# Optimization experiments

Hardware: AMD Instinct MI355X
Metric: run time of the kernel (lower is better)

The kernel has to match this reference:

```python
import jax, jax.numpy as jnp
import numpy as np

B, N, IC, PC, OUT = 2, 4096, 256, 128, 128
BN_EPS = 1e-5


def setup_inputs() -> dict:
    key = jax.random.key(0)
    ks = jax.random.split(key, 6)
    return {
        "point_features": jax.random.normal(ks[0], (B, PC, N), jnp.float32),
        "img_features": jax.random.normal(ks[1], (B, IC, N), jnp.float32),
        "fc2_w": jax.random.normal(ks[2], (PC, IC), jnp.float32) * (1.0 / np.sqrt(IC)),
        "fc2_b": jax.random.normal(ks[3], (PC,), jnp.float32) * 0.01,
        "conv_w": jax.random.normal(ks[4], (OUT, 2 * PC), jnp.float32) * (1.0 / np.sqrt(2 * PC)),
        "conv_b": jax.random.normal(ks[5], (OUT,), jnp.float32) * 0.01,
        "bn_gamma": jnp.ones((OUT,), jnp.float32),
        "bn_beta": jnp.zeros((OUT,), jnp.float32),
        "bn_mean": jnp.zeros((OUT,), jnp.float32),
        "bn_var": jnp.ones((OUT,), jnp.float32),
    }


def reference(point_features, img_features, fc2_w, fc2_b, conv_w, conv_b,
              bn_gamma, bn_beta, bn_mean, bn_var):
    # IA_layer3 (dropout in eval mode -> identity)
    rp = jnp.swapaxes(point_features, 1, 2)            # [B, N, pc]
    ri = jnp.swapaxes(img_features, 1, 2) @ fc2_w.T + fc2_b  # fc2: [B, N, pc]
    scale = 1.0 / np.sqrt(PC).astype(np.float32)

    # scores = rp @ ri^T / sqrt(d); softmax over dim=1 (the rp-token axis)
    s_p = jnp.einsum('bnd,bmd->bnm', rp, ri) * scale   # [B, N, N]
    aw_p = jax.nn.softmax(s_p, axis=1)
    out_p = jnp.einsum('bij,bjd->bid', aw_p, rp)       # [B, N, pc]

    s_i = jnp.einsum('bnd,bmd->bnm', ri, rp) * scale   # [B, N, N]
    aw_i = jax.nn.softmax(s_i, axis=1)
    out_i = jnp.einsum('bij,bjd->bid', aw_i, ri)       # [B, N, pc]

    # fuse: permute to channel-first, concat on channels -> [B, 2*pc, N]
    fusion = jnp.concatenate([jnp.swapaxes(out_p, 1, 2),
                              jnp.swapaxes(out_i, 1, 2)], axis=1)
    # conv1d(k=1) + BN(eval) + ReLU, all per-channel elementwise over N
    y = jnp.einsum('oc,bcn->bon', conv_w, fusion) + conv_b[None, :, None]
    inv_std = jax.lax.rsqrt(bn_var + BN_EPS)
    y = (y - bn_mean[None, :, None]) * (bn_gamma * inv_std)[None, :, None] \
        + bn_beta[None, :, None]
    return jax.nn.relu(y)                              # [B, OUT, N]
```

## Files before the change

### kernel.cpp

```cpp
#include <hip/hip_runtime.h>
#include <math.h>

#define NTOK 4096
#define PCH  128
#define ICH  256
#define OCH  128
#define NB   2
#define SCALEF 0.08838834764831845f

typedef __bf16 bf16_t;
typedef __attribute__((ext_vector_type(8))) __bf16 bf16x8;
typedef __attribute__((ext_vector_type(4))) __bf16 bf16x4;
typedef __attribute__((ext_vector_type(4))) float floatx4;

#define LDK 136
#define LDJ 72

__global__ __launch_bounds__(256) void pack_all(const float* __restrict__ pf,
                                                const float* __restrict__ img,
                                                bf16_t* __restrict__ pfC,
                                                bf16_t* __restrict__ pfT,
                                                bf16_t* __restrict__ imgT)
{
    __shared__ float Ls[64][65];
    const int t = threadIdx.x;
    const int n0 = blockIdx.x * 64, b = blockIdx.z;
    const bool ispf = blockIdx.y < 2;
    const int d0 = ispf ? blockIdx.y * 64 : (blockIdx.y - 2) * 64;
    const float* src = (ispf ? pf + ((size_t)(b * PCH + d0)) * NTOK
                             : img + ((size_t)(b * ICH + d0)) * NTOK) + n0;
#pragma unroll
    for (int p = 0; p < 4; p++) {
        int d = p * 16 + (t >> 4), c = t & 15;
        float4 v = *(const float4*)&src[d * NTOK + c * 4];
        Ls[d][c * 4 + 0] = v.x; Ls[d][c * 4 + 1] = v.y;
        Ls[d][c * 4 + 2] = v.z; Ls[d][c * 4 + 3] = v.w;
        if (ispf) {
            bf16x4 o = { (bf16_t)v.x, (bf16_t)v.y, (bf16_t)v.z, (bf16_t)v.w };
            *(bf16x4*)&pfC[((size_t)(b * PCH + d0 + d)) * NTOK + n0 + c * 4] = o;
        }
    }
    __syncthreads();
#pragma unroll
    for (int p = 0; p < 2; p++) {
        int n = p * 32 + (t >> 3), c = t & 7;
        bf16x8 o;
#pragma unroll
        for (int k = 0; k < 8; k++) o[k] = (bf16_t)Ls[c * 8 + k][n];
        if (ispf)
            *(bf16x8*)&pfT[((size_t)(b * NTOK + n0 + n)) * PCH + d0 + c * 8] = o;
        else
            *(bf16x8*)&imgT[((size_t)(b * NTOK + n0 + n)) * ICH + d0 + c * 8] = o;
    }
}

__global__ __launch_bounds__(256) void fc2_mfma(const bf16_t* __restrict__ imgT,
                                                const float* __restrict__ w,
                                                const float* __restrict__ bias,
                                                bf16_t* __restrict__ riC,
                                                bf16_t* __restrict__ riT,
                                                float* __restrict__ zsums)
{
    const int t = threadIdx.x;
    if (blockIdx.y == 0 && blockIdx.z == 0)
        zsums[blockIdx.x * 256 + t] = 0.f;

    const int n0 = blockIdx.x * 64, pbase = blockIdx.y * 64, b = blockIdx.z;
    const int lane = t & 63, wv = t >> 6, tx = lane & 15, q = lane >> 4;
    const int n = n0 + wv * 16 + tx;
    const bf16_t* trow = imgT + ((size_t)(b * NTOK + n)) * ICH;

    floatx4 acc[4];
#pragma unroll
    for (int ot = 0; ot < 4; ot++) acc[ot] = (floatx4){0.f, 0.f, 0.f, 0.f};

#pragma unroll
    for (int s = 0; s < 8; s++) {
        bf16x8 bf = *(const bf16x8*)&trow[s * 32 + q * 8];
#pragma unroll
        for (int ot = 0; ot < 4; ot++) {
            const float* wr = w + (size_t)(pbase + ot * 16 + tx) * ICH + s * 32 + q * 8;
            float4 x0 = *(const float4*)wr;
            float4 x1 = *(const float4*)(wr + 4);
            bf16x8 af;
            af[0] = (bf16_t)x0.x; af[1] = (bf16_t)x0.y; af[2] = (bf16_t)x0.z; af[3] = (bf16_t)x0.w;
            af[4] = (bf16_t)x1.x; af[5] = (bf16_t)x1.y; af[6] = (bf16_t)x1.z; af[7] = (bf16_t)x1.w;
            acc[ot] = __builtin_amdgcn_mfma_f32_16x16x32_bf16(af, bf, acc[ot], 0, 0, 0);
        }
    }

#pragma unroll
    for (int ot = 0; ot < 4; ot++) {
        bf16x4 tv;
#pragma unroll
        for (int r = 0; r < 4; r++) {
            const int p = pbase + ot * 16 + q * 4 + r;
            float v = acc[ot][r] + bias[p];
            tv[r] = (bf16_t)v;
            riC[((size_t)(b * PCH + p)) * NTOK + n] = (bf16_t)v;
        }
        *(bf16x4*)&riT[((size_t)(b * NTOK + n)) * PCH + pbase + ot * 16 + q * 4] = tv;
    }
}

__global__ __launch_bounds__(256, 4) void stats_mfma(const bf16_t* __restrict__ pfT,
                                                     const bf16_t* __restrict__ riT,
                                                     float* __restrict__ zr,
                                                     float* __restrict__ zc,
                                                     float* __restrict__ fus)
{
    __shared__ bf16_t As[64 * LDK];
    __shared__ float zacc[1024];
    const int t = threadIdx.x;
    const int blk = blockIdx.x;

    {
        float4* f4 = (float4*)fus + ((size_t)blk * 256 + t) * 4;
        f4[0] = float4{0.f, 0.f, 0.f, 0.f};
        f4[1] = float4{0.f, 0.f, 0.f, 0.f};
        f4[2] = float4{0.f, 0.f, 0.f, 0.f};
        f4[3] = float4{0.f, 0.f, 0.f, 0.f};
    }

    const int g = blk & 7, slot = blk >> 3;
    const int b = g & 1, js = g >> 1;
    const bf16_t* At = pfT + (size_t)b * NTOK * PCH;
    const bf16_t* Bt = riT + (size_t)b * NTOK * PCH;
    float* zrow = zr + (size_t)b * NTOK;
    float* zcol = zc + (size_t)b * NTOK;
    const int lane = t & 63, w = t >> 6, tx = lane & 15, q = lane >> 4;
    const int i0 = slot * 64;
    const int jbase = js * 1024;
    const int sr = t >> 4, sc = t & 15;
    const bf16_t* Brow = Bt + (size_t)(jbase + w * 16 + tx) * PCH;

    bf16x8 bcur[4];
#pragma unroll
    for (int s = 0; s < 4; s++)
        bcur[s] = *(const bf16x8*)&Brow[s * 32 + q * 8];
#pragma unroll
    for (int p = 0; p < 4; p++) {
        int i = p * 16 + sr;
        *(uint4*)&As[i * LDK + sc * 8] = *(const uint4*)&At[((size_t)(i0 + i)) * PCH + sc * 8];
    }
    __syncthreads();
    bf16x8 af[4][4];
#pragma unroll
    for (int mt = 0; mt < 4; mt++)
#pragma unroll
        for (int s = 0; s < 4; s++)
            af[mt][s] = *(bf16x8*)&As[(mt * 16 + tx) * LDK + s * 32 + q * 8];

    float racc[4] = {0.f, 0.f, 0.f, 0.f};
    for (int jt = 0; jt < 16; jt++) {
        __builtin_amdgcn_s_barrier();
        floatx4 sacc[4];
#pragma unroll
        for (int mt = 0; mt < 4; mt++) {
            sacc[mt] = (floatx4){0.f, 0.f, 0.f, 0.f};
#pragma unroll
            for (int s = 0; s < 4; s++)
                sacc[mt] = __builtin_amdgcn_mfma_f32_16x16x32_bf16(bcur[s], af[mt][s], sacc[mt], 0, 0, 0);
        }
        if (jt < 15) {
            const bf16_t* bn = Brow + (size_t)(jt + 1) * 64 * PCH;
#pragma unroll
            for (int s = 0; s < 4; s++)
                bcur[s] = *(const bf16x8*)&bn[s * 32 + q * 8];
        }

        float ctmp[4] = {0.f, 0.f, 0.f, 0.f};
#pragma unroll
        for (int mt = 0; mt < 4; mt++)
#pragma unroll
            for (int r = 0; r < 4; r++) {
                float e = __expf(sacc[mt][r] * SCALEF);
                racc[mt] += e;
                ctmp[r]  += e;
            }
#pragma unroll
        for (int r = 0; r < 4; r++) {
            float v = ctmp[r];
            v += __shfl_xor(v, 1); v += __shfl_xor(v, 2);
            v += __shfl_xor(v, 4); v += __shfl_xor(v, 8);
            if (tx == 0) zacc[jt * 64 + w * 16 + q * 4 + r] = v;
        }
    }
#pragma unroll
    for (int mt = 0; mt < 4; mt++) {
        float v = racc[mt];
        v += __shfl_xor(v, 16);
        v += __shfl_xor(v, 32);
        if (q == 0) atomicAdd(&zrow[i0 + mt * 16 + tx], v);
    }
    __syncthreads();
#pragma unroll
    for (int k = 0; k < 4; k++)
        atomicAdd(&zcol[jbase + k * 256 + t], zacc[k * 256 + t]);
}

__global__ __launch_bounds__(256, 3) void attn_mfma(const bf16_t* __restrict__ pfT,
                                                    const bf16_t* __restrict__ riT,
                                                    const bf16_t* __restrict__ pfC,
                                                    const bf16_t* __restrict__ riC,
                                                    const float* __restrict__ zrsum,
                                                    const float* __restrict__ zcsum,
                                                    float* __restrict__ fus)
{
    __shared__ bf16_t As[64 * LDK];
    __shared__ bf16_t Es[2][64 * LDJ];
    const int t = threadIdx.x;
    const int blk = blockIdx.x;
    const int g = (blk & 7) * 2 + ((blk >> 3) >> 6);
    const int slot = (blk >> 3) & 63;
    const int b = g & 1, z = g >> 1;
    const int mode = z >> 2, js = z & 3;
    const bf16_t* At = (mode == 0 ? pfT : riT) + (size_t)b * NTOK * PCH;
    const bf16_t* Bt = (mode == 0 ? riT : pfT) + (size_t)b * NTOK * PCH;
    const bf16_t* Vc = (mode == 0 ? pfC : riC) + (size_t)b * PCH * NTOK;
    const float* wsum = (mode == 0 ? zcsum : zrsum) + (size_t)b * NTOK;
    const int lane = t & 63, w = t >> 6, tx = lane & 15, q = lane >> 4;
    const int i0 = slot * 64;
    const int jbase = js * 1024;
    const int sr = t >> 4, sc = t & 15;
    const bf16_t* Brow = Bt + (size_t)(jbase + w * 16 + tx) * PCH;

    bf16x8 bcur[4];
#pragma unroll
    for (int s = 0; s < 4; s++)
        bcur[s] = *(const bf16x8*)&Brow[s * 32 + q * 8];
    bf16x8 vcur[2][2];
#pragma unroll
    for (int nt = 0; nt < 2; nt++)
#pragma unroll
        for (int s = 0; s < 2; s++)
            vcur[nt][s] = *(const bf16x8*)&Vc[((size_t)(w * 32 + nt * 16 + tx)) * NTOK + jbase + s * 32 + q * 8];
    float4 wv = *(const float4*)&wsum[jbase + w * 16 + q * 4];
    float4 wr4 = {1.f / wv.x, 1.f / wv.y, 1.f / wv.z, 1.f / wv.w};

#pragma unroll
    for (int p = 0; p < 4; p++) {
        int i = p * 16 + sr;
        *(uint4*)&As[i * LDK + sc * 8] = *(const uint4*)&At[((size_t)(i0 + i)) * PCH + sc * 8];
    }
    __syncthreads();
    bf16x8 af[4][4];
#pragma unroll
    for (int mt = 0; mt < 4; mt++)
#pragma unroll
        for (int s = 0; s < 4; s++)
            af[mt][s] = *(bf16x8*)&As[(mt * 16 + tx) * LDK + s * 32 + q * 8];

    floatx4 outacc[4][2];
#pragma unroll
    for (int mt = 0; mt < 4; mt++)
#pragma unroll
        for (int nt = 0; nt < 2; nt++)
            outacc[mt][nt] = (floatx4){0.f, 0.f, 0.f, 0.f};

    for (int jt = 0; jt < 16; jt++) {
        const int cur = jt & 1;
        const int j0 = jbase + jt * 64;

        floatx4 sacc[4];
#pragma unroll
        for (int mt = 0; mt < 4; mt++) {
            sacc[mt] = (floatx4){0.f, 0.f, 0.f, 0.f};
#pragma unroll
            for (int s = 0; s < 4; s++)
                sacc[mt] = __builtin_amdgcn_mfma_f32_16x16x32_bf16(bcur[s], af[mt][s], sacc[mt], 0, 0, 0);
        }
        if (jt < 15) {
            const bf16_t* bn = Brow + (size_t)(jt + 1) * 64 * PCH;
#pragma unroll
            for (int s = 0; s < 4; s++)
                bcur[s] = *(const bf16x8*)&bn[s * 32 + q * 8];
        }

#pragma unroll
        for (int mt = 0; mt < 4; mt++) {
            bf16x4 ev;
#pragma unroll
            for (int r = 0; r < 4; r++)
                ev[r] = (bf16_t)(__expf(sacc[mt][r] * SCALEF) * ((const float*)&wr4)[r]);
            *(bf16x4*)&Es[cur][(mt * 16 + tx) * LDJ + w * 16 + q * 4] = ev;
        }
        float4 wnv;
        if (jt < 15)
            wnv = *(const float4*)&wsum[j0 + 64 + w * 16 + q * 4];

        __syncthreads();

        bf16x8 ef[4][2];
#pragma unroll
        for (int mt = 0; mt < 4; mt++)
#pragma unroll
            for (int s = 0; s < 2; s++)
                ef[mt][s] = *(bf16x8*)&Es[cur][(mt * 16 + tx) * LDJ + s * 32 + q * 8];
#pragma unroll
        for (int nt = 0; nt < 2; nt++)
#pragma unroll
            for (int s = 0; s < 2; s++)
#pragma unroll
                for (int mt = 0; mt < 4; mt++)
                    outacc[mt][nt] = __builtin_amdgcn_mfma_f32_16x16x32_bf16(ef[mt][s], vcur[nt][s], outacc[mt][nt], 0, 0, 0);

        if (jt < 15) {
#pragma unroll
            for (int nt = 0; nt < 2; nt++)
#pragma unroll
                for (int s = 0; s < 2; s++)
                    vcur[nt][s] = *(const bf16x8*)&Vc[((size_t)(w * 32 + nt * 16 + tx)) * NTOK + (j0 + 64) + s * 32 + q * 8];
            wr4 = (float4){1.f / wnv.x, 1.f / wnv.y, 1.f / wnv.z, 1.f / wnv.w};
        }
    }

    float* fo = fus + ((size_t)(b * NTOK + i0)) * 256 + mode * 128 + w * 32;
#pragma unroll
    for (int mt = 0; mt < 4; mt++)
#pragma unroll
        for (int nt = 0; nt < 2; nt++)
#pragma unroll
            for (int r = 0; r < 4; r++)
                atomicAdd(&fo[(mt * 16 + q * 4 + r) * 256 + nt * 16 + tx], outacc[mt][nt][r]);
}

__global__ __launch_bounds__(256) void conv_mfma(const float* __restrict__ fus,
                                                 const float* __restrict__ cw,
                                                 const float* __restrict__ cb,
                                                 const float* __restrict__ g,
                                                 const float* __restrict__ be,
                                                 const float* __restrict__ mu,
                                                 const float* __restrict__ var,
                                                 float* __restrict__ out)
{
    const int t = threadIdx.x;
    const int n0 = blockIdx.x * 64, obase = blockIdx.y * 64, b = blockIdx.z;
    const int lane = t & 63, wv = t >> 6, tx = lane & 15, q = lane >> 4;
    const int n = n0 + wv * 16 + tx;
    const float* frow = fus + ((size_t)(b * NTOK + n)) * 256;

    floatx4 acc[4];
#pragma unroll
    for (int ot = 0; ot < 4; ot++) acc[ot] = (floatx4){0.f, 0.f, 0.f, 0.f};

#pragma unroll
    for (int s = 0; s < 8; s++) {
        float4 f0 = *(const float4*)&frow[s * 32 + q * 8];
        float4 f1 = *(const float4*)&frow[s * 32 + q * 8 + 4];
        bf16x8 bf;
        bf[0] = (bf16_t)f0.x; bf[1] = (bf16_t)f0.y; bf[2] = (bf16_t)f0.z; bf[3] = (bf16_t)f0.w;
        bf[4] = (bf16_t)f1.x; bf[5] = (bf16_t)f1.y; bf[6] = (bf16_t)f1.z; bf[7] = (bf16_t)f1.w;
#pragma unroll
        for (int ot = 0; ot < 4; ot++) {
            const float* wr = cw + (size_t)(obase + ot * 16 + tx) * 256 + s * 32 + q * 8;
            float4 x0 = *(const float4*)wr;
            float4 x1 = *(const float4*)(wr + 4);
            bf16x8 af;
            af[0] = (bf16_t)x0.x; af[1] = (bf16_t)x0.y; af[2] = (bf16_t)x0.z; af[3] = (bf16_t)x0.w;
            af[4] = (bf16_t)x1.x; af[5] = (bf16_t)x1.y; af[6] = (bf16_t)x1.z; af[7] = (bf16_t)x1.w;
            acc[ot] = __builtin_amdgcn_mfma_f32_16x16x32_bf16(af, bf, acc[ot], 0, 0, 0);
        }
    }

#pragma unroll
    for (int ot = 0; ot < 4; ot++)
#pragma unroll
        for (int r = 0; r < 4; r++) {
            const int o = obase + ot * 16 + q * 4 + r;
            const float sc = g[o] * rsqrtf(var[o] + 1e-5f);
            const float b0 = be[o] + (cb[o] - mu[o]) * sc;
            float y = acc[ot][r] * sc + b0;
            out[((size_t)(b * OCH + o)) * NTOK + n] = fmaxf(y, 0.f);
        }
}

extern "C" void kernel_launch(void* const* d_in, const int* in_sizes, int n_in,
                              void* d_out, int out_size, void* d_ws, size_t ws_size,
                              hipStream_t stream)
{
    const float* pf   = (const float*)d_in[0];
    const float* img  = (const float*)d_in[1];
    const float* fc2w = (const float*)d_in[2];
    const float* fc2b = (const float*)d_in[3];
    const float* cw   = (const float*)d_in[4];
    const float* cb   = (const float*)d_in[5];
    const float* g    = (const float*)d_in[6];
    const float* be   = (const float*)d_in[7];
    const float* mu   = (const float*)d_in[8];
    const float* var  = (const float*)d_in[9];
    float* out = (float*)d_out;

    float* fus   = (float*)d_ws;
    float* zrsum = fus + (size_t)NB * NTOK * 256;
    float* zcsum = zrsum + NB * NTOK;
    bf16_t* pfC = (bf16_t*)(zcsum + NB * NTOK);
    bf16_t* pfT = pfC + (size_t)NB * PCH * NTOK;
    bf16_t* riC = pfT + (size_t)NB * NTOK * PCH;
    bf16_t* riT = riC + (size_t)NB * PCH * NTOK;
    bf16_t* imgT = (bf16_t*)fus;

    pack_all  <<<dim3(64, 6, NB), 256, 0, stream>>>(pf, img, pfC, pfT, imgT);
    fc2_mfma  <<<dim3(64, 2, NB), 256, 0, stream>>>(imgT, fc2w, fc2b, riC, riT, zrsum);
    stats_mfma<<<dim3(512),       256, 0, stream>>>(pfT, riT, zrsum, zcsum, fus);
    attn_mfma <<<dim3(1024),      256, 0, stream>>>(pfT, riT, pfC, riC, zrsum, zcsum, fus);
    conv_mfma <<<dim3(64, 2, NB), 256, 0, stream>>>(fus, cw, cb, g, be, mu, var, out);
}
```

Baseline: 212.6 us.

## Keep attention probabilities in registers and split j across waves in attn kernel

Restructures the attention kernel so each wave computes its own score tile and feeds the exponentiated probabilities straight into the PV MFMA from registers, dropping the LDS round trip and the per-tile barrier. Each block now covers 2048 j columns with a 2x2 wave split over rows and j, and the grid is halved. The exponent uses exp2 with the log of the column sum folded in, and MFMA phases are wrapped in setprio. Partial outputs from the two j halves are reduced in LDS before global atomics, at the cost of more registers (occupancy hint lowered to 2) and a longer reduction epilogue.

```diff
diff --git a/kernel.cpp b/kernel.cpp
--- a/kernel.cpp
+++ b/kernel.cpp
@@ -7,6 +7,7 @@
 #define OCH  128
 #define NB   2
 #define SCALEF 0.08838834764831845f
+#define SCALE2 0.12751743f
 
 typedef __bf16 bf16_t;
 typedef __attribute__((ext_vector_type(8))) __bf16 bf16x8;
@@ -14,7 +15,6 @@
 typedef __attribute__((ext_vector_type(4))) float floatx4;
 
 #define LDK 136
-#define LDJ 72
 
 __global__ __launch_bounds__(256) void pack_all(const float* __restrict__ pf,
                                                 const float* __restrict__ img,
@@ -199,7 +199,7 @@
         atomicAdd(&zcol[jbase + k * 256 + t], zacc[k * 256 + t]);
 }
 
-__global__ __launch_bounds__(256, 3) void attn_mfma(const bf16_t* __restrict__ pfT,
+__global__ __launch_bounds__(256, 2) void attn_mfma(const bf16_t* __restrict__ pfT,
                                                     const bf16_t* __restrict__ riT,
                                                     const bf16_t* __restrict__ pfC,
                                                     const bf16_t* __restrict__ riC,
@@ -207,36 +207,22 @@
                                                     const float* __restrict__ zcsum,
                                                     float* __restrict__ fus)
 {
-    __shared__ bf16_t As[64 * LDK];
-    __shared__ bf16_t Es[2][64 * LDJ];
+    __shared__ float Rs[4352];
+    bf16_t* As = (bf16_t*)Rs;
     const int t = threadIdx.x;
     const int blk = blockIdx.x;
-    const int g = (blk & 7) * 2 + ((blk >> 3) >> 6);
-    const int slot = (blk >> 3) & 63;
-    const int b = g & 1, z = g >> 1;
-    const int mode = z >> 2, js = z & 3;
+    const int g = blk & 7;
+    const int slot = blk >> 3;
+    const int b = g & 1, mode = (g >> 1) & 1, js = g >> 2;
     const bf16_t* At = (mode == 0 ? pfT : riT) + (size_t)b * NTOK * PCH;
     const bf16_t* Bt = (mode == 0 ? riT : pfT) + (size_t)b * NTOK * PCH;
     const bf16_t* Vc = (mode == 0 ? pfC : riC) + (size_t)b * PCH * NTOK;
     const float* wsum = (mode == 0 ? zcsum : zrsum) + (size_t)b * NTOK;
     const int lane = t & 63, w = t >> 6, tx = lane & 15, q = lane >> 4;
+    const int h = w & 1, jh = w >> 1;
     const int i0 = slot * 64;
-    const int jbase = js * 1024;
+    const int jbase = js * 2048;
     const int sr = t >> 4, sc = t & 15;
-    const bf16_t* Brow = Bt + (size_t)(jbase + w * 16 + tx) * PCH;
-
-    bf16x8 bcur[4];
-#pragma unroll
-    for (int s = 0; s < 4; s++)
-        bcur[s] = *(const bf16x8*)&Brow[s * 32 + q * 8];
-    bf16x8 vcur[2][2];
-#pragma unroll
-    for (int nt = 0; nt < 2; nt++)
-#pragma unroll
-        for (int s = 0; s < 2; s++)
-            vcur[nt][s] = *(const bf16x8*)&Vc[((size_t)(w * 32 + nt * 16 + tx)) * NTOK + jbase + s * 32 + q * 8];
-    float4 wv = *(const float4*)&wsum[jbase + w * 16 + q * 4];
-    float4 wr4 = {1.f / wv.x, 1.f / wv.y, 1.f / wv.z, 1.f / wv.w};
 
 #pragma unroll
     for (int p = 0; p < 4; p++) {
@@ -244,85 +230,120 @@
         *(uint4*)&As[i * LDK + sc * 8] = *(const uint4*)&At[((size_t)(i0 + i)) * PCH + sc * 8];
     }
     __syncthreads();
-    bf16x8 af[4][4];
-#pragma unroll
-    for (int mt = 0; mt < 4; mt++)
+    bf16x8 af[2][4];
+#pragma unroll
+    for (int mt = 0; mt < 2; mt++)
 #pragma unroll
         for (int s = 0; s < 4; s++)
-            af[mt][s] = *(bf16x8*)&As[(mt * 16 + tx) * LDK + s * 32 + q * 8];
-
-    floatx4 outacc[4][2];
-#pragma unroll
-    for (int mt = 0; mt < 4; mt++)
-#pragma unroll
-        for (int nt = 0; nt < 2; nt++)
-            outacc[mt][nt] = (floatx4){0.f, 0.f, 0.f, 0.f};
-
-    for (int jt = 0; jt < 16; jt++) {
-        const int cur = jt & 1;
-        const int j0 = jbase + jt * 64;
-
-        floatx4 sacc[4];
-#pragma unroll
-        for (int mt = 0; mt < 4; mt++) {
-            sacc[mt] = (floatx4){0.f, 0.f, 0.f, 0.f};
-#pragma unroll
-            for (int s = 0; s < 4; s++)
-                sacc[mt] = __builtin_amdgcn_mfma_f32_16x16x32_bf16(bcur[s], af[mt][s], sacc[mt], 0, 0, 0);
-        }
-        if (jt < 15) {
-            const bf16_t* bn = Brow + (size_t)(jt + 1) * 64 * PCH;
-#pragma unroll
-            for (int s = 0; s < 4; s++)
-                bcur[s] = *(const bf16x8*)&bn[s * 32 + q * 8];
-        }
-
-#pragma unroll
-        for (int mt = 0; mt < 4; mt++) {
-            bf16x4 ev;
-#pragma unroll
-            for (int r = 0; r < 4; r++)
-                ev[r] = (bf16_t)(__expf(sacc[mt][r] * SCALEF) * ((const float*)&wr4)[r]);
-            *(bf16x4*)&Es[cur][(mt * 16 + tx) * LDJ + w * 16 + q * 4] = ev;
-        }
-        float4 wnv;
-        if (jt < 15)
-            wnv = *(const float4*)&wsum[j0 + 64 + w * 16 + q * 4];
-
+            af[mt][s] = *(bf16x8*)&As[(h * 32 + mt * 16 + tx) * LDK + s * 32 + q * 8];
+
+    const bf16_t* Brow0 = Bt + (size_t)(jbase + jh * 32 + tx) * PCH;
+    const bf16_t* Vrow  = Vc + (size_t)tx * NTOK + jbase + jh * 32 + q * 4;
+    const float*  Wp    = wsum + jbase + jh * 32 + q * 4;
+
+    floatx4 acc[2][8];
+#pragma unroll
+    for (int mt = 0; mt < 2; mt++)
+#pragma unroll
+        for (int c = 0; c < 8; c++) acc[mt][c] = (floatx4){0.f, 0.f, 0.f, 0.f};
+
+    bf16x8 bcur[2][4];
+#pragma unroll
+    for (int jm = 0; jm < 2; jm++)
+#pragma unroll
+        for (int s = 0; s < 4; s++)
+            bcur[jm][s] = *(const bf16x8*)&Brow0[(size_t)(jm * 16) * PCH + s * 32 + q * 8];
+    bf16x8 vcur[8];
+#pragma unroll
+    for (int c = 0; c < 8; c++) {
+        ((bf16x4*)&vcur[c])[0] = *(const bf16x4*)&Vrow[(size_t)(c * 16) * NTOK];
+        ((bf16x4*)&vcur[c])[1] = *(const bf16x4*)&Vrow[(size_t)(c * 16) * NTOK + 16];
+    }
+    float4 wv0 = *(const float4*)&Wp[0];
+    float4 wv1 = *(const float4*)&Wp[16];
+
+#pragma unroll 1
+    for (int jt = 0; jt < 32; jt++) {
+        __builtin_amdgcn_s_setprio(1);
+        floatx4 sx[2][2];
+#pragma unroll
+        for (int jm = 0; jm < 2; jm++)
+#pragma unroll
+            for (int mt = 0; mt < 2; mt++) {
+                sx[jm][mt] = (floatx4){0.f, 0.f, 0.f, 0.f};
+#pragma unroll
+                for (int s = 0; s < 4; s++)
+                    sx[jm][mt] = __builtin_amdgcn_mfma_f32_16x16x32_bf16(bcur[jm][s], af[mt][s], sx[jm][mt], 0, 0, 0);
+            }
+        __builtin_amdgcn_s_setprio(0);
+
+        if (jt < 31) {
+            const bf16_t* bn = Brow0 + (size_t)((jt + 1) * 64) * PCH;
+#pragma unroll
+            for (int jm = 0; jm < 2; jm++)
+#pragma unroll
+                for (int s = 0; s < 4; s++)
+                    bcur[jm][s] = *(const bf16x8*)&bn[(size_t)(jm * 16) * PCH + s * 32 + q * 8];
+        }
+
+        float lz0[4] = { __builtin_amdgcn_logf(wv0.x), __builtin_amdgcn_logf(wv0.y),
+                         __builtin_amdgcn_logf(wv0.z), __builtin_amdgcn_logf(wv0.w) };
+        float lz1[4] = { __builtin_amdgcn_logf(wv1.x), __builtin_amdgcn_logf(wv1.y),
+                         __builtin_amdgcn_logf(wv1.z), __builtin_amdgcn_logf(wv1.w) };
+        bf16x8 ea[2];
+#pragma unroll
+        for (int mt = 0; mt < 2; mt++)
+#pragma unroll
+            for (int r = 0; r < 4; r++) {
+                ea[mt][r]     = (bf16_t)__builtin_amdgcn_exp2f(sx[0][mt][r] * SCALE2 - lz0[r]);
+                ea[mt][r + 4] = (bf16_t)__builtin_amdgcn_exp2f(sx[1][mt][r] * SCALE2 - lz1[r]);
+            }
+        if (jt < 31) {
+            wv0 = *(const float4*)&Wp[(jt + 1) * 64];
+            wv1 = *(const float4*)&Wp[(jt + 1) * 64 + 16];
+        }
+
+        __builtin_amdgcn_s_setprio(1);
+#pragma unroll
+        for (int c = 0; c < 8; c++)
+#pragma unroll
+            for (int mt = 0; mt < 2; mt++)
+                acc[mt][c] = __builtin_amdgcn_mfma_f32_16x16x32_bf16(ea[mt], vcur[c], acc[mt][c], 0, 0, 0);
+        __builtin_amdgcn_s_setprio(0);
+
+        if (jt < 31) {
+            const bf16_t* vn = Vrow + (jt + 1) * 64;
+#pragma unroll
+            for (int c = 0; c < 8; c++) {
+                ((bf16x4*)&vcur[c])[0] = *(const bf16x4*)&vn[(size_t)(c * 16) * NTOK];
+                ((bf16x4*)&vcur[c])[1] = *(const bf16x4*)&vn[(size_t)(c * 16) * NTOK + 16];
+            }
+        }
+    }
+
+    __syncthreads();
+#pragma unroll
+    for (int half = 0; half < 2; half++) {
+        for (int k = t; k < 64 * 65; k += 256) Rs[k] = 0.f;
         __syncthreads();
-
-        bf16x8 ef[4][2];
-#pragma unroll
-        for (int mt = 0; mt < 4; mt++)
-#pragma unroll
-            for (int s = 0; s < 2; s++)
-                ef[mt][s] = *(bf16x8*)&Es[cur][(mt * 16 + tx) * LDJ + s * 32 + q * 8];
-#pragma unroll
-        for (int nt = 0; nt < 2; nt++)
-#pragma unroll
-            for (int s = 0; s < 2; s++)
-#pragma unroll
-                for (int mt = 0; mt < 4; mt++)
-                    outacc[mt][nt] = __builtin_amdgcn_mfma_f32_16x16x32_bf16(ef[mt][s], vcur[nt][s], outacc[mt][nt], 0, 0, 0);
-
-        if (jt < 15) {
-#pragma unroll
-            for (int nt = 0; nt < 2; nt++)
-#pragma unroll
-                for (int s = 0; s < 2; s++)
-                    vcur[nt][s] = *(const bf16x8*)&Vc[((size_t)(w * 32 + nt * 16 + tx)) * NTOK + (j0 + 64) + s * 32 + q * 8];
-            wr4 = (float4){1.f / wnv.x, 1.f / wnv.y, 1.f / wnv.z, 1.f / wnv.w};
-        }
-    }
-
-    float* fo = fus + ((size_t)(b * NTOK + i0)) * 256 + mode * 128 + w * 32;
-#pragma unroll
-    for (int mt = 0; mt < 4; mt++)
-#pragma unroll
-        for (int nt = 0; nt < 2; nt++)
-#pragma unroll
-            for (int r = 0; r < 4; r++)
-                atomicAdd(&fo[(mt * 16 + q * 4 + r) * 256 + nt * 16 + tx], outacc[mt][nt][r]);
+#pragma unroll
+        for (int mt = 0; mt < 2; mt++)
+#pragma unroll
+            for (int c = 0; c < 4; c++)
+#pragma unroll
+                for (int r = 0; r < 4; r++)
+                    atomicAdd(&Rs[(h * 32 + mt * 16 + q * 4 + r) * 65 + c * 16 + tx],
+                              acc[mt][half * 4 + c][r]);
+        __syncthreads();
+        {
+            const int il = t >> 2, d0 = (t & 3) * 16;
+            float* fo = fus + ((size_t)(b * NTOK + i0 + il)) * 256 + mode * 128 + half * 64 + d0;
+#pragma unroll
+            for (int k = 0; k < 16; k++)
+                atomicAdd(&fo[k], Rs[il * 65 + d0 + k]);
+        }
+        __syncthreads();
+    }
 }
 
 __global__ __launch_bounds__(256) void conv_mfma(const float* __restrict__ fus,
@@ -403,6 +424,6 @@
     pack_all  <<<dim3(64, 6, NB), 256, 0, stream>>>(pf, img, pfC, pfT, imgT);
     fc2_mfma  <<<dim3(64, 2, NB), 256, 0, stream>>>(imgT, fc2w, fc2b, riC, riT, zrsum);
     stats_mfma<<<dim3(512),       256, 0, stream>>>(pfT, riT, zrsum, zcsum, fus);
-    attn_mfma <<<dim3(1024),      256, 0, stream>>>(pfT, riT, pfC, riC, zrsum, zcsum, fus);
+    attn_mfma <<<dim3(512),       256, 0, stream>>>(pfT, riT, pfC, riC, zrsum, zcsum, fus);
     conv_mfma <<<dim3(64, 2, NB), 256, 0, stream>>>(fus, cw, cb, g, be, mu, var, out);
 }
```

Result: slower. 497.3 us (+133.9%).
